# Optimization experiments

Measured on AMD Instinct MI355X. Metric: run time of the kernel, lower is better.

## Reference

```python
import jax, jax.numpy as jnp
import numpy as np

B, S, E, H, D = 4, 2048, 2048, 16, 128
EPS = 1e-6


def _rope_cache(seq_len, dim, base=10000.0):
    # standard rotary cache, half-split layout matching rotate_half
    inv_freq = 1.0 / (base ** (np.arange(0, dim // 2, dtype=np.float32) / (dim // 2)))
    t = np.arange(seq_len, dtype=np.float32)
    freqs = np.outer(t, inv_freq)                     # [S, D/2]
    emb = np.concatenate([freqs, freqs], axis=-1)     # [S, D]
    cos = jnp.asarray(np.cos(emb))[None, :, None, :]  # [1, S, 1, D]
    sin = jnp.asarray(np.sin(emb))[None, :, None, :]
    return cos, sin


def setup_inputs() -> dict:
    key = jax.random.key(0)
    ks = jax.random.split(key, 5)
    scale = 1.0 / np.sqrt(E)
    x = jax.random.normal(ks[0], (B, S, E), dtype=jnp.float32)
    Wq = jax.random.normal(ks[1], (E, E), dtype=jnp.float32) * scale
    Wk = jax.random.normal(ks[2], (E, E), dtype=jnp.float32) * scale
    Wv = jax.random.normal(ks[3], (E, E), dtype=jnp.float32) * scale
    Wo = jax.random.normal(ks[4], (E, E), dtype=jnp.float32) * scale
    cos, sin = _rope_cache(S, D)
    return {"x": x, "cos": cos, "sin": sin, "Wq": Wq, "Wk": Wk, "Wv": Wv, "Wo": Wo}


def _rotate_half(t):
    d = t.shape[-1] // 2
    return jnp.concatenate([-t[..., d:], t[..., :d]], axis=-1)


def _rms_norm(t, eps):
    return t * jax.lax.rsqrt(jnp.mean(t * t, axis=-1, keepdims=True) + eps)


def reference(x, cos, sin, Wq, Wk, Wv, Wo):
    b, s, _ = x.shape
    # QKV projections (Linear without bias: x @ W.T), reshape to heads
    q = (x @ Wq.T).reshape(b, s, H, D)
    k = (x @ Wk.T).reshape(b, s, H, D)
    v = (x @ Wv.T).reshape(b, s, H, D)
    # RoPE then QK RMSNorm (no learned scale)
    q = _rms_norm(q * cos + _rotate_half(q) * sin, EPS)
    k = _rms_norm(k * cos + _rotate_half(k) * sin, EPS)
    # non-causal SDPA
    scores = jnp.einsum("bqhd,bkhd->bhqk", q, k) / np.sqrt(D)
    probs = jax.nn.softmax(scores, axis=-1)
    y = jnp.einsum("bhqk,bkhd->bqhd", probs, v).reshape(b, s, H * D)
    return y @ Wo.T
```

## Files before the change

### kernel.cpp

```cpp
#include <hip/hip_runtime.h>
#include <hip/hip_bf16.h>
#include <math.h>


typedef __bf16 bf16_t;
typedef __bf16 bf16x2 __attribute__((ext_vector_type(2)));
typedef __bf16 bf16x4 __attribute__((ext_vector_type(4)));
typedef __bf16 bf16x8 __attribute__((ext_vector_type(8)));
typedef float f32x2 __attribute__((ext_vector_type(2)));
typedef float f32x4 __attribute__((ext_vector_type(4)));
typedef float f32x16 __attribute__((ext_vector_type(16)));
typedef unsigned int u32;
typedef u32 u32x4 __attribute__((ext_vector_type(4)));

typedef __attribute__((address_space(1))) const void gas_cvoid;
typedef __attribute__((address_space(3))) void las_void;

#define MFMA16(a, b, c) __builtin_amdgcn_mfma_f32_16x16x32_bf16((a), (b), (c), 0, 0, 0)
#define MFMA32(a, b, c) __builtin_amdgcn_mfma_f32_32x32x16_bf16((a), (b), (c), 0, 0, 0)

__device__ __forceinline__ void gload16(const void* g, void* l) {
  __builtin_amdgcn_global_load_lds((gas_cvoid*)g, (las_void*)l, 16, 0, 0);
}
__device__ __forceinline__ void pl32(u32& a, u32& b) {
  asm volatile("v_permlane32_swap_b32 %0, %1" : "+v"(a), "+v"(b));
}
__device__ __forceinline__ float fexp2(float x) {
  float r;
  asm("v_exp_f32 %0, %1" : "=v"(r) : "v"(x));
  return r;
}

__global__ __launch_bounds__(256) void cvt_bf16(const float* __restrict__ in,
                                                bf16_t* __restrict__ out) {
  const size_t i = ((size_t)blockIdx.x * 256 + threadIdx.x) * 4;
  f32x4 v = *(const f32x4*)&in[i];
  bf16x4 o;
#pragma unroll
  for (int j = 0; j < 4; ++j) o[j] = (bf16_t)v[j];
  *(bf16x4*)&out[i] = o;
}
__global__ __launch_bounds__(256) void cvt_w4(const float* __restrict__ w0,
                                              const float* __restrict__ w1,
                                              const float* __restrict__ w2,
                                              const float* __restrict__ w3,
                                              bf16_t* __restrict__ o0,
                                              bf16_t* __restrict__ o1,
                                              bf16_t* __restrict__ o2,
                                              bf16_t* __restrict__ o3) {
  const int which = blockIdx.x >> 12;
  const float* in = which == 0 ? w0 : which == 1 ? w1 : which == 2 ? w2 : w3;
  bf16_t* out = which == 0 ? o0 : which == 1 ? o1 : which == 2 ? o2 : o3;
  const size_t i = ((size_t)(blockIdx.x & 4095) * 256 + threadIdx.x) * 4;
  f32x4 v = *(const f32x4*)&in[i];
  bf16x4 o;
#pragma unroll
  for (int j = 0; j < 4; ++j) o[j] = (bf16_t)v[j];
  *(bf16x4*)&out[i] = o;
}

template <int MODE, typename CT, int NT_T>
__global__ __launch_bounds__(512, 2) void gemm8(const bf16_t* __restrict__ A,
                                                const bf16_t* __restrict__ Bt,
                                                CT* __restrict__ C) {
  constexpr int K = 2048;
  __shared__ __attribute__((aligned(16))) char lds[131072];
  const int tid = threadIdx.x;
  const int wave = tid >> 6, lane = tid & 63;
  const int bid = blockIdx.x;
  const int swz = (bid & 7) * 32 + (bid >> 3);
  const int m0 = (swz / NT_T) * 256, n0 = (swz % NT_T) * 256;

  const int srow = tid >> 3;
  const int scol = ((tid & 7) ^ (srow & 7)) * 8;
  const bf16_t* aBase = A + (size_t)(m0 + srow) * K + scol;
  const bf16_t* bBase = Bt + (size_t)(n0 + srow) * K + scol;

  const int wm = wave >> 2, wn = wave & 3;
  const int l15 = lane & 15, l4 = lane >> 4;
  const int axor = l15 & 7;
  char* const wdst = lds + wave * 1024;

  f32x4 acc[8][4] = {};

  gload16(bBase, wdst + 32768);
  gload16(bBase + (size_t)64 * K, wdst + 32768 + 8192);
  gload16(bBase + (size_t)128 * K, wdst + 32768 + 16384);
  gload16(bBase + (size_t)192 * K, wdst + 32768 + 24576);
  gload16(aBase, wdst);
  gload16(aBase + (size_t)128 * K, wdst + 16384);
  gload16(aBase + (size_t)64 * K, wdst + 8192);
  gload16(aBase + (size_t)192 * K, wdst + 24576);

  for (int t = 0; t < 32; ++t) {
    const int buf = t & 1, nbuf = buf ^ 1;
    const char* la = lds + buf * 65536 + wm * 16384;
    const char* lb = lds + buf * 65536 + 32768 + (wn >> 1) * 16384 + (wn & 1) * 8192;
    char* const ndst = wdst + nbuf * 65536;
    bf16x8 bF[4][2];
#pragma unroll
    for (int q = 0; q < 4; ++q) {
      if (q == 0) {
        asm volatile("s_waitcnt vmcnt(2)" ::: "memory");
      } else if (q == 2) {
        if (t < 31)
          asm volatile("s_waitcnt vmcnt(4)" ::: "memory");
        else
          asm volatile("s_waitcnt vmcnt(0)" ::: "memory");
      }
      __builtin_amdgcn_s_barrier();

      bf16x8 aF[2][2];
#pragma unroll
      for (int dm = 0; dm < 2; ++dm)
#pragma unroll
        for (int kk = 0; kk < 2; ++kk)
          aF[dm][kk] = *(const bf16x8*)(la + ((q * 2 + dm) * 16 + l15) * 128 +
                                        ((kk * 4 + l4) ^ axor) * 16);
      if (q == 0) {
#pragma unroll
        for (int ni = 0; ni < 4; ++ni)
#pragma unroll
          for (int kk = 0; kk < 2; ++kk)
            bF[ni][kk] = *(const bf16x8*)(lb + (ni * 16 + l15) * 128 +
                                          ((kk * 4 + l4) ^ axor) * 16);
      }
      if (t < 31) {
        const int off = (t + 1) * 64;
        if (q == 0) {
          gload16(bBase + off, ndst + 32768);
          gload16(bBase + (size_t)64 * K + off, ndst + 32768 + 8192);
        } else if (q == 1) {
          gload16(bBase + (size_t)128 * K + off, ndst + 32768 + 16384);
          gload16(bBase + (size_t)192 * K + off, ndst + 32768 + 24576);
        } else if (q == 2) {
          gload16(aBase + off, ndst);
          gload16(aBase + (size_t)128 * K + off, ndst + 16384);
        } else {
          gload16(aBase + (size_t)64 * K + off, ndst + 8192);
          gload16(aBase + (size_t)192 * K + off, ndst + 24576);
        }
      }
      __builtin_amdgcn_s_setprio(1);
#pragma unroll
      for (int kk = 0; kk < 2; ++kk)
#pragma unroll
        for (int dm = 0; dm < 2; ++dm)
#pragma unroll
          for (int ni = 0; ni < 4; ++ni)
            acc[q * 2 + dm][ni] = MFMA16(aF[dm][kk], bF[ni][kk], acc[q * 2 + dm][ni]);
      __builtin_amdgcn_s_setprio(0);
    }
  }

  const int rBase = m0 + wm * 128 + l4 * 4;
  const int cBase = n0 + wn * 64 + l15;
#pragma unroll
  for (int mi = 0; mi < 8; ++mi)
#pragma unroll
    for (int ni = 0; ni < 4; ++ni)
#pragma unroll
      for (int j = 0; j < 4; ++j) {
        const int r = rBase + mi * 16 + j;
        const int c = cBase + ni * 16;
        const CT v = (CT)acc[mi][ni][j];
        if (MODE == 0) {
          const int b = r >> 11, s = r & 2047, hh = c >> 7, d = c & 127;
          C[(((size_t)(b * 16 + hh)) * 2048 + s) * 128 + d] = v;
        } else if (MODE == 1) {
          C[(size_t)r * 2048 + c] = v;
        } else {
          const int hh = r >> 7, dd = r & 127, b = c >> 11, s = c & 2047;
          C[((size_t)(b * 16 + hh) * 128 + dd) * 2048 + s] = v;
        }
      }
}

__global__ __launch_bounds__(256) void rope_rms(bf16_t* __restrict__ T,
                                                const float* __restrict__ Cs,
                                                const float* __restrict__ Sn) {
  const int wave = threadIdx.x >> 6, lane = threadIdx.x & 63;
#pragma unroll 1
  for (int rr = 0; rr < 8; ++rr) {
    const size_t row = (size_t)blockIdx.x * 32 + wave * 8 + rr;
    const int s = (int)(row & 2047);
    bf16_t* p = &T[row * 128 + 2 * lane];
    const float a0 = (float)p[0], a1 = (float)p[1];
    f32x2 cv = *(const f32x2*)&Cs[(size_t)s * 128 + 2 * lane];
    f32x2 sv = *(const f32x2*)&Sn[(size_t)s * 128 + 2 * lane];
    const float p0 = __shfl_xor(a0, 32);
    const float p1 = __shfl_xor(a1, 32);
    const float sg = (lane < 32) ? -1.f : 1.f;
    const float r0 = a0 * cv.x + sg * p0 * sv.x;
    const float r1 = a1 * cv.y + sg * p1 * sv.y;
    float ss = r0 * r0 + r1 * r1;
#pragma unroll
    for (int off = 1; off < 64; off <<= 1) ss += __shfl_xor(ss, off);
    const float inv = rsqrtf(ss * (1.0f / 128.0f) + 1e-6f);
    p[0] = (bf16_t)(r0 * inv);
    p[1] = (bf16_t)(r1 * inv);
  }
}

__global__ __launch_bounds__(512, 2) void attn_fwd(const bf16_t* __restrict__ Q,
                                                   const bf16_t* __restrict__ K,
                                                   const bf16_t* __restrict__ Vt,
                                                   bf16_t* __restrict__ Y) {
  __shared__ __attribute__((aligned(16))) bf16_t ldsK[2][64 * 128];
  __shared__ __attribute__((aligned(16))) bf16_t ldsV[2][128 * 64];
  const int tid = threadIdx.x, wave = tid >> 6, lane = tid & 63;
  const int l31 = lane & 31, hi = lane >> 5;
  const int pid = blockIdx.x;
  const int bh = (pid & 7) * 8 + ((pid >> 3) & 7);
  const int qb = pid >> 6;
  const int b = bh >> 4, h = bh & 15;
  const bf16_t* Qh = Q + (size_t)bh * 2048 * 128;
  const bf16_t* Kh = K + (size_t)bh * 2048 * 128;
  const bf16_t* Vh = Vt + (size_t)bh * 128 * 2048;
  const int q0 = qb * 256 + wave * 32;

  bf16x8 qf[8];
#pragma unroll
  for (int dk = 0; dk < 8; ++dk)
    qf[dk] = *(const bf16x8*)&Qh[(size_t)(q0 + l31) * 128 + dk * 16 + hi * 8];

  f32x16 ot[4] = {};
  float l_r = 0.f;
  const float SC2 = 0.08838834764831845f * 1.44269504088896341f;
  const float NC2 = -11.5f * 1.44269504088896341f;

  auto stage = [&](int kt, int bu) {
#pragma unroll
    for (int i = 0; i < 2; ++i) {
      const int G = wave * 64 + lane + i * 512;
      char* dstK = (char*)&ldsK[bu][0] + (wave * 64 + i * 512) * 16;
      char* dstV = (char*)&ldsV[bu][0] + (wave * 64 + i * 512) * 16;
      const int kvr = G >> 4, glk = G & 15;
      gload16(Kh + (size_t)(kt * 64 + kvr) * 128 + ((glk ^ (kvr & 7)) * 8), dstK);
      const int dr = G >> 3, glv = G & 7;
      gload16(Vh + (size_t)dr * 2048 + kt * 64 + ((glv ^ (dr & 7)) * 8), dstV);
    }
  };

  stage(0, 0);
  stage(1, 1);
  asm volatile("s_waitcnt vmcnt(4)" ::: "memory");
  __builtin_amdgcn_s_barrier();
  __builtin_amdgcn_sched_barrier(0);

  for (int kt = 0; kt < 32; ++kt) {
    const int bu = kt & 1;
    const int r7 = l31 & 7;

    f32x16 sa0 = {}, sa1 = {};
    __builtin_amdgcn_s_setprio(1);
#pragma unroll
    for (int dk = 0; dk < 8; ++dk) {
      const int g = ((dk << 1) | hi) ^ r7;
      bf16x8 kf0 = *(const bf16x8*)&ldsK[bu][l31 * 128 + g * 8];
      bf16x8 kf1 = *(const bf16x8*)&ldsK[bu][(32 + l31) * 128 + g * 8];
      sa0 = MFMA32(kf0, qf[dk], sa0);
      sa1 = MFMA32(kf1, qf[dk], sa1);
    }
    __builtin_amdgcn_s_setprio(0);

    u32 w[2][8];
    float ssum = 0.f;
#pragma unroll
    for (int i = 0; i < 8; ++i) {
      const float p0 = fexp2(fmaf(sa0[2 * i], SC2, NC2));
      const float p1 = fexp2(fmaf(sa0[2 * i + 1], SC2, NC2));
      const float p2 = fexp2(fmaf(sa1[2 * i], SC2, NC2));
      const float p3 = fexp2(fmaf(sa1[2 * i + 1], SC2, NC2));
      ssum += (p0 + p1) + (p2 + p3);
      bf16x2 t0, t1;
      t0[0] = (bf16_t)p0; t0[1] = (bf16_t)p1;
      t1[0] = (bf16_t)p2; t1[1] = (bf16_t)p3;
      w[0][i] = __builtin_bit_cast(u32, t0);
      w[1][i] = __builtin_bit_cast(u32, t1);
    }
    ssum += __shfl_xor(ssum, 32);
    l_r += ssum;

#pragma unroll
    for (int ks = 0; ks < 4; ++ks) {
      const int tsel = ks >> 1, k4 = (ks & 1) * 4;
      u32 a0 = w[tsel][k4 + 0], b0 = w[tsel][k4 + 2];
      u32 a1 = w[tsel][k4 + 1], b1 = w[tsel][k4 + 3];
      pl32(a0, b0);
      pl32(a1, b1);
      u32x4 fw;
      fw.x = a0; fw.y = a1; fw.z = b0; fw.w = b1;
      const bf16x8 pf = __builtin_bit_cast(bf16x8, fw);
      const int gv = ((ks << 1) | hi) ^ r7;
      __builtin_amdgcn_s_setprio(1);
#pragma unroll
      for (int db = 0; db < 4; ++db) {
        bf16x8 vf = *(const bf16x8*)&ldsV[bu][(db * 32 + l31) * 64 + gv * 8];
        ot[db] = MFMA32(vf, pf, ot[db]);
      }
      __builtin_amdgcn_s_setprio(0);
    }

    __builtin_amdgcn_s_barrier();
    __builtin_amdgcn_sched_barrier(0);
    if (kt < 30) {
      stage(kt + 2, bu);
      asm volatile("s_waitcnt vmcnt(4)" ::: "memory");
    } else {
      asm volatile("s_waitcnt vmcnt(0)" ::: "memory");
    }
    __builtin_amdgcn_s_barrier();
    __builtin_amdgcn_sched_barrier(0);
  }

  const float rl = 1.f / l_r;
  const size_t yrow = ((size_t)(b * 2048 + q0 + l31) * 16 + h) * 128;
#pragma unroll
  for (int db = 0; db < 4; ++db)
#pragma unroll
    for (int g2 = 0; g2 < 4; ++g2) {
      bf16x4 ov;
#pragma unroll
      for (int j = 0; j < 4; ++j) ov[j] = (bf16_t)(ot[db][g2 * 4 + j] * rl);
      *(bf16x4*)&Y[yrow + db * 32 + g2 * 8 + hi * 4] = ov;
    }
}

extern "C" void kernel_launch(void* const* d_in, const int* in_sizes, int n_in,
                              void* d_out, int out_size, void* d_ws, size_t ws_size,
                              hipStream_t stream) {
  const float* x = (const float*)d_in[0];
  const float* cs = (const float*)d_in[1];
  const float* sn = (const float*)d_in[2];
  const float* Wq = (const float*)d_in[3];
  const float* Wk = (const float*)d_in[4];
  const float* Wv = (const float*)d_in[5];
  const float* Wo = (const float*)d_in[6];

  bf16_t* ws = (bf16_t*)d_ws;
  const size_t TSZ = (size_t)4 * 2048 * 2048;
  const size_t WSZ = (size_t)2048 * 2048;
  bf16_t* xb = ws;
  bf16_t* Wqb = ws + TSZ;
  bf16_t* Wkb = Wqb + WSZ;
  bf16_t* Wvb = Wkb + WSZ;
  bf16_t* Wob = Wvb + WSZ;
  bf16_t* Qb = ws + 2 * TSZ;
  bf16_t* Kb = Qb + TSZ;
  bf16_t* Vtb = Kb + TSZ;
  bf16_t* Yb = xb;

  cvt_bf16<<<16384, 256, 0, stream>>>(x, xb);
  cvt_w4<<<16384, 256, 0, stream>>>(Wq, Wk, Wv, Wo, Wqb, Wkb, Wvb, Wob);

  gemm8<0, bf16_t, 8><<<256, 512, 0, stream>>>(xb, Wqb, Qb);
  gemm8<0, bf16_t, 8><<<256, 512, 0, stream>>>(xb, Wkb, Kb);
  gemm8<2, bf16_t, 32><<<256, 512, 0, stream>>>(Wvb, xb, Vtb);
  rope_rms<<<4096, 256, 0, stream>>>(Qb, cs, sn);
  rope_rms<<<4096, 256, 0, stream>>>(Kb, cs, sn);
  attn_fwd<<<512, 512, 0, stream>>>(Qb, Kb, Vtb, Yb);
  gemm8<1, float, 8><<<256, 512, 0, stream>>>(Yb, Wob, (float*)d_out);
}
```

Baseline: 476.3 us.

## Process two query tiles per attention block and fuse the Q/K RoPE launches

The attention kernel now gives each wave two 32-row query tiles, 256 rows apart. It reuses every K and V fragment read from LDS for both tiles and halves the grid to 256 blocks of 512 threads. This halves the global-to-LDS K/V staging traffic and LDS reads per unit of work. The cost is roughly double the accumulator and Q registers, and the min-blocks launch bound is dropped, so each CU runs fewer resident waves to hide latency. Separately, the two RoPE+RMSNorm launches are merged into one launch with an 8192-block grid that picks Q or K by block index, saving one kernel launch.

```diff
diff --git a/kernel.cpp b/kernel.cpp
--- a/kernel.cpp
+++ b/kernel.cpp
@@ -176,13 +176,16 @@
       }
 }
 
-__global__ __launch_bounds__(256) void rope_rms(bf16_t* __restrict__ T,
-                                                const float* __restrict__ Cs,
-                                                const float* __restrict__ Sn) {
+__global__ __launch_bounds__(256) void rope_rms2(bf16_t* __restrict__ Qb,
+                                                 bf16_t* __restrict__ Kb,
+                                                 const float* __restrict__ Cs,
+                                                 const float* __restrict__ Sn) {
+  bf16_t* T = (blockIdx.x >> 12) ? Kb : Qb;
+  const int bid = blockIdx.x & 4095;
   const int wave = threadIdx.x >> 6, lane = threadIdx.x & 63;
 #pragma unroll 1
   for (int rr = 0; rr < 8; ++rr) {
-    const size_t row = (size_t)blockIdx.x * 32 + wave * 8 + rr;
+    const size_t row = (size_t)bid * 32 + wave * 8 + rr;
     const int s = (int)(row & 2047);
     bf16_t* p = &T[row * 128 + 2 * lane];
     const float a0 = (float)p[0], a1 = (float)p[1];
@@ -202,10 +205,10 @@
   }
 }
 
-__global__ __launch_bounds__(512, 2) void attn_fwd(const bf16_t* __restrict__ Q,
-                                                   const bf16_t* __restrict__ K,
-                                                   const bf16_t* __restrict__ Vt,
-                                                   bf16_t* __restrict__ Y) {
+__global__ __launch_bounds__(512) void attn_fwd(const bf16_t* __restrict__ Q,
+                                                const bf16_t* __restrict__ K,
+                                                const bf16_t* __restrict__ Vt,
+                                                bf16_t* __restrict__ Y) {
   __shared__ __attribute__((aligned(16))) bf16_t ldsK[2][64 * 128];
   __shared__ __attribute__((aligned(16))) bf16_t ldsV[2][128 * 64];
   const int tid = threadIdx.x, wave = tid >> 6, lane = tid & 63;
@@ -217,15 +220,17 @@
   const bf16_t* Qh = Q + (size_t)bh * 2048 * 128;
   const bf16_t* Kh = K + (size_t)bh * 2048 * 128;
   const bf16_t* Vh = Vt + (size_t)bh * 128 * 2048;
-  const int q0 = qb * 256 + wave * 32;
-
-  bf16x8 qf[8];
-#pragma unroll
-  for (int dk = 0; dk < 8; ++dk)
-    qf[dk] = *(const bf16x8*)&Qh[(size_t)(q0 + l31) * 128 + dk * 16 + hi * 8];
-
-  f32x16 ot[4] = {};
-  float l_r = 0.f;
+  const int q0 = qb * 512 + wave * 32;
+
+  bf16x8 qfA[8], qfB[8];
+#pragma unroll
+  for (int dk = 0; dk < 8; ++dk) {
+    qfA[dk] = *(const bf16x8*)&Qh[(size_t)(q0 + l31) * 128 + dk * 16 + hi * 8];
+    qfB[dk] = *(const bf16x8*)&Qh[(size_t)(q0 + 256 + l31) * 128 + dk * 16 + hi * 8];
+  }
+
+  f32x16 otA[4] = {}, otB[4] = {};
+  float lA = 0.f, lB = 0.f;
   const float SC2 = 0.08838834764831845f * 1.44269504088896341f;
   const float NC2 = -11.5f * 1.44269504088896341f;
 
@@ -252,52 +257,77 @@
     const int bu = kt & 1;
     const int r7 = l31 & 7;
 
-    f32x16 sa0 = {}, sa1 = {};
+    f32x16 sa0A = {}, sa1A = {}, sa0B = {}, sa1B = {};
     __builtin_amdgcn_s_setprio(1);
 #pragma unroll
     for (int dk = 0; dk < 8; ++dk) {
       const int g = ((dk << 1) | hi) ^ r7;
       bf16x8 kf0 = *(const bf16x8*)&ldsK[bu][l31 * 128 + g * 8];
       bf16x8 kf1 = *(const bf16x8*)&ldsK[bu][(32 + l31) * 128 + g * 8];
-      sa0 = MFMA32(kf0, qf[dk], sa0);
-      sa1 = MFMA32(kf1, qf[dk], sa1);
+      sa0A = MFMA32(kf0, qfA[dk], sa0A);
+      sa1A = MFMA32(kf1, qfA[dk], sa1A);
+      sa0B = MFMA32(kf0, qfB[dk], sa0B);
+      sa1B = MFMA32(kf1, qfB[dk], sa1B);
     }
     __builtin_amdgcn_s_setprio(0);
 
-    u32 w[2][8];
-    float ssum = 0.f;
+    u32 wA[2][8], wB[2][8];
+    float ssA = 0.f, ssB = 0.f;
 #pragma unroll
     for (int i = 0; i < 8; ++i) {
-      const float p0 = fexp2(fmaf(sa0[2 * i], SC2, NC2));
-      const float p1 = fexp2(fmaf(sa0[2 * i + 1], SC2, NC2));
-      const float p2 = fexp2(fmaf(sa1[2 * i], SC2, NC2));
-      const float p3 = fexp2(fmaf(sa1[2 * i + 1], SC2, NC2));
-      ssum += (p0 + p1) + (p2 + p3);
+      const float p0 = fexp2(fmaf(sa0A[2 * i], SC2, NC2));
+      const float p1 = fexp2(fmaf(sa0A[2 * i + 1], SC2, NC2));
+      const float p2 = fexp2(fmaf(sa1A[2 * i], SC2, NC2));
+      const float p3 = fexp2(fmaf(sa1A[2 * i + 1], SC2, NC2));
+      ssA += (p0 + p1) + (p2 + p3);
       bf16x2 t0, t1;
       t0[0] = (bf16_t)p0; t0[1] = (bf16_t)p1;
       t1[0] = (bf16_t)p2; t1[1] = (bf16_t)p3;
-      w[0][i] = __builtin_bit_cast(u32, t0);
-      w[1][i] = __builtin_bit_cast(u32, t1);
-    }
-    ssum += __shfl_xor(ssum, 32);
-    l_r += ssum;
+      wA[0][i] = __builtin_bit_cast(u32, t0);
+      wA[1][i] = __builtin_bit_cast(u32, t1);
+    }
+#pragma unroll
+    for (int i = 0; i < 8; ++i) {
+      const float p0 = fexp2(fmaf(sa0B[2 * i], SC2, NC2));
+      const float p1 = fexp2(fmaf(sa0B[2 * i + 1], SC2, NC2));
+      const float p2 = fexp2(fmaf(sa1B[2 * i], SC2, NC2));
+      const float p3 = fexp2(fmaf(sa1B[2 * i + 1], SC2, NC2));
+      ssB += (p0 + p1) + (p2 + p3);
+      bf16x2 t0, t1;
+      t0[0] = (bf16_t)p0; t0[1] = (bf16_t)p1;
+      t1[0] = (bf16_t)p2; t1[1] = (bf16_t)p3;
+      wB[0][i] = __builtin_bit_cast(u32, t0);
+      wB[1][i] = __builtin_bit_cast(u32, t1);
+    }
+    ssA += __shfl_xor(ssA, 32);
+    ssB += __shfl_xor(ssB, 32);
+    lA += ssA;
+    lB += ssB;
 
 #pragma unroll
     for (int ks = 0; ks < 4; ++ks) {
       const int tsel = ks >> 1, k4 = (ks & 1) * 4;
-      u32 a0 = w[tsel][k4 + 0], b0 = w[tsel][k4 + 2];
-      u32 a1 = w[tsel][k4 + 1], b1 = w[tsel][k4 + 3];
+      u32 a0 = wA[tsel][k4 + 0], b0 = wA[tsel][k4 + 2];
+      u32 a1 = wA[tsel][k4 + 1], b1 = wA[tsel][k4 + 3];
       pl32(a0, b0);
       pl32(a1, b1);
-      u32x4 fw;
-      fw.x = a0; fw.y = a1; fw.z = b0; fw.w = b1;
-      const bf16x8 pf = __builtin_bit_cast(bf16x8, fw);
+      u32x4 fwA;
+      fwA.x = a0; fwA.y = a1; fwA.z = b0; fwA.w = b1;
+      const bf16x8 pfA = __builtin_bit_cast(bf16x8, fwA);
+      u32 c0 = wB[tsel][k4 + 0], d0 = wB[tsel][k4 + 2];
+      u32 c1 = wB[tsel][k4 + 1], d1 = wB[tsel][k4 + 3];
+      pl32(c0, d0);
+      pl32(c1, d1);
+      u32x4 fwB;
+      fwB.x = c0; fwB.y = c1; fwB.z = d0; fwB.w = d1;
+      const bf16x8 pfB = __builtin_bit_cast(bf16x8, fwB);
       const int gv = ((ks << 1) | hi) ^ r7;
       __builtin_amdgcn_s_setprio(1);
 #pragma unroll
       for (int db = 0; db < 4; ++db) {
         bf16x8 vf = *(const bf16x8*)&ldsV[bu][(db * 32 + l31) * 64 + gv * 8];
-        ot[db] = MFMA32(vf, pf, ot[db]);
+        otA[db] = MFMA32(vf, pfA, otA[db]);
+        otB[db] = MFMA32(vf, pfB, otB[db]);
       }
       __builtin_amdgcn_s_setprio(0);
     }
@@ -314,16 +344,21 @@
     __builtin_amdgcn_sched_barrier(0);
   }
 
-  const float rl = 1.f / l_r;
-  const size_t yrow = ((size_t)(b * 2048 + q0 + l31) * 16 + h) * 128;
+  const float rlA = 1.f / lA, rlB = 1.f / lB;
+  const size_t yrA = ((size_t)(b * 2048 + q0 + l31) * 16 + h) * 128;
+  const size_t yrB = ((size_t)(b * 2048 + q0 + 256 + l31) * 16 + h) * 128;
 #pragma unroll
   for (int db = 0; db < 4; ++db)
 #pragma unroll
     for (int g2 = 0; g2 < 4; ++g2) {
-      bf16x4 ov;
-#pragma unroll
-      for (int j = 0; j < 4; ++j) ov[j] = (bf16_t)(ot[db][g2 * 4 + j] * rl);
-      *(bf16x4*)&Y[yrow + db * 32 + g2 * 8 + hi * 4] = ov;
+      bf16x4 ovA, ovB;
+#pragma unroll
+      for (int j = 0; j < 4; ++j) {
+        ovA[j] = (bf16_t)(otA[db][g2 * 4 + j] * rlA);
+        ovB[j] = (bf16_t)(otB[db][g2 * 4 + j] * rlB);
+      }
+      *(bf16x4*)&Y[yrA + db * 32 + g2 * 8 + hi * 4] = ovA;
+      *(bf16x4*)&Y[yrB + db * 32 + g2 * 8 + hi * 4] = ovB;
     }
 }
 
@@ -357,8 +392,7 @@
   gemm8<0, bf16_t, 8><<<256, 512, 0, stream>>>(xb, Wqb, Qb);
   gemm8<0, bf16_t, 8><<<256, 512, 0, stream>>>(xb, Wkb, Kb);
   gemm8<2, bf16_t, 32><<<256, 512, 0, stream>>>(Wvb, xb, Vtb);
-  rope_rms<<<4096, 256, 0, stream>>>(Qb, cs, sn);
-  rope_rms<<<4096, 256, 0, stream>>>(Kb, cs, sn);
-  attn_fwd<<<512, 512, 0, stream>>>(Qb, Kb, Vtb, Yb);
+  rope_rms2<<<8192, 256, 0, stream>>>(Qb, Kb, cs, sn);
+  attn_fwd<<<256, 512, 0, stream>>>(Qb, Kb, Vtb, Yb);
   gemm8<1, float, 8><<<256, 512, 0, stream>>>(Yb, Wob, (float*)d_out);
 }
```

Result: slower. 749.6 us (+57.4%).

## Switch GEMM to 32x32x16 MFMA tiles and merge Q/K rope kernels

Applied to the files above, without the earlier changes.

Each wave of the GEMM now computes its 128x64 tile with 32x32x16 bf16 MFMA instructions (4x2 f32x16 accumulators) in place of 16x16x32 ones. LDS fragment loads and the epilogue index mapping are rewritten to match the 32-row lane layout. The larger instruction should cut issue overhead and LDS fragment reads per FLOP, at the cost of a different epilogue store pattern. The two rope_rms launches for Q and K are also merged into one 8192-block launch to save a kernel launch.

```diff
diff --git a/kernel.cpp b/kernel.cpp
--- a/kernel.cpp
+++ b/kernel.cpp
@@ -16,7 +16,6 @@
 typedef __attribute__((address_space(1))) const void gas_cvoid;
 typedef __attribute__((address_space(3))) void las_void;
 
-#define MFMA16(a, b, c) __builtin_amdgcn_mfma_f32_16x16x32_bf16((a), (b), (c), 0, 0, 0)
 #define MFMA32(a, b, c) __builtin_amdgcn_mfma_f32_32x32x16_bf16((a), (b), (c), 0, 0, 0)
 
 __device__ __forceinline__ void gload16(const void* g, void* l) {
@@ -77,11 +76,11 @@
   const bf16_t* bBase = Bt + (size_t)(n0 + srow) * K + scol;
 
   const int wm = wave >> 2, wn = wave & 3;
-  const int l15 = lane & 15, l4 = lane >> 4;
-  const int axor = l15 & 7;
+  const int l31 = lane & 31, hi = lane >> 5;
+  const int axor = l31 & 7;
   char* const wdst = lds + wave * 1024;
 
-  f32x4 acc[8][4] = {};
+  f32x16 acc[4][2] = {};
 
   gload16(bBase, wdst + 32768);
   gload16(bBase + (size_t)64 * K, wdst + 32768 + 8192);
@@ -97,7 +96,7 @@
     const char* la = lds + buf * 65536 + wm * 16384;
     const char* lb = lds + buf * 65536 + 32768 + (wn >> 1) * 16384 + (wn & 1) * 8192;
     char* const ndst = wdst + nbuf * 65536;
-    bf16x8 bF[4][2];
+    bf16x8 bF[2][4];
 #pragma unroll
     for (int q = 0; q < 4; ++q) {
       if (q == 0) {
@@ -110,20 +109,18 @@
       }
       __builtin_amdgcn_s_barrier();
 
-      bf16x8 aF[2][2];
-#pragma unroll
-      for (int dm = 0; dm < 2; ++dm)
-#pragma unroll
-        for (int kk = 0; kk < 2; ++kk)
-          aF[dm][kk] = *(const bf16x8*)(la + ((q * 2 + dm) * 16 + l15) * 128 +
-                                        ((kk * 4 + l4) ^ axor) * 16);
+      bf16x8 aF[4];
+#pragma unroll
+      for (int kk = 0; kk < 4; ++kk)
+        aF[kk] = *(const bf16x8*)(la + (q * 32 + l31) * 128 +
+                                  ((kk * 2 + hi) ^ axor) * 16);
       if (q == 0) {
 #pragma unroll
-        for (int ni = 0; ni < 4; ++ni)
-#pragma unroll
-          for (int kk = 0; kk < 2; ++kk)
-            bF[ni][kk] = *(const bf16x8*)(lb + (ni * 16 + l15) * 128 +
-                                          ((kk * 4 + l4) ^ axor) * 16);
+        for (int nt = 0; nt < 2; ++nt)
+#pragma unroll
+          for (int kk = 0; kk < 4; ++kk)
+            bF[nt][kk] = *(const bf16x8*)(lb + (nt * 32 + l31) * 128 +
+                                          ((kk * 2 + hi) ^ axor) * 16);
       }
       if (t < 31) {
         const int off = (t + 1) * 64;
@@ -143,27 +140,25 @@
       }
       __builtin_amdgcn_s_setprio(1);
 #pragma unroll
-      for (int kk = 0; kk < 2; ++kk)
-#pragma unroll
-        for (int dm = 0; dm < 2; ++dm)
-#pragma unroll
-          for (int ni = 0; ni < 4; ++ni)
-            acc[q * 2 + dm][ni] = MFMA16(aF[dm][kk], bF[ni][kk], acc[q * 2 + dm][ni]);
+      for (int kk = 0; kk < 4; ++kk)
+#pragma unroll
+        for (int nt = 0; nt < 2; ++nt)
+          acc[q][nt] = MFMA32(aF[kk], bF[nt][kk], acc[q][nt]);
       __builtin_amdgcn_s_setprio(0);
     }
   }
 
-  const int rBase = m0 + wm * 128 + l4 * 4;
-  const int cBase = n0 + wn * 64 + l15;
-#pragma unroll
-  for (int mi = 0; mi < 8; ++mi)
-#pragma unroll
-    for (int ni = 0; ni < 4; ++ni)
-#pragma unroll
-      for (int j = 0; j < 4; ++j) {
-        const int r = rBase + mi * 16 + j;
-        const int c = cBase + ni * 16;
-        const CT v = (CT)acc[mi][ni][j];
+  const int rBase = m0 + wm * 128 + 4 * hi;
+  const int cBase = n0 + wn * 64 + l31;
+#pragma unroll
+  for (int mt = 0; mt < 4; ++mt)
+#pragma unroll
+    for (int nt = 0; nt < 2; ++nt)
+#pragma unroll
+      for (int j = 0; j < 16; ++j) {
+        const int r = rBase + mt * 32 + (j & 3) + 8 * (j >> 2);
+        const int c = cBase + nt * 32;
+        const CT v = (CT)acc[mt][nt][j];
         if (MODE == 0) {
           const int b = r >> 11, s = r & 2047, hh = c >> 7, d = c & 127;
           C[(((size_t)(b * 16 + hh)) * 2048 + s) * 128 + d] = v;
@@ -176,13 +171,16 @@
       }
 }
 
-__global__ __launch_bounds__(256) void rope_rms(bf16_t* __restrict__ T,
-                                                const float* __restrict__ Cs,
-                                                const float* __restrict__ Sn) {
+__global__ __launch_bounds__(256) void rope_rms2(bf16_t* __restrict__ Qb,
+                                                 bf16_t* __restrict__ Kb,
+                                                 const float* __restrict__ Cs,
+                                                 const float* __restrict__ Sn) {
+  bf16_t* T = (blockIdx.x >> 12) ? Kb : Qb;
+  const int bid = blockIdx.x & 4095;
   const int wave = threadIdx.x >> 6, lane = threadIdx.x & 63;
 #pragma unroll 1
   for (int rr = 0; rr < 8; ++rr) {
-    const size_t row = (size_t)blockIdx.x * 32 + wave * 8 + rr;
+    const size_t row = (size_t)bid * 32 + wave * 8 + rr;
     const int s = (int)(row & 2047);
     bf16_t* p = &T[row * 128 + 2 * lane];
     const float a0 = (float)p[0], a1 = (float)p[1];
@@ -357,8 +355,7 @@
   gemm8<0, bf16_t, 8><<<256, 512, 0, stream>>>(xb, Wqb, Qb);
   gemm8<0, bf16_t, 8><<<256, 512, 0, stream>>>(xb, Wkb, Kb);
   gemm8<2, bf16_t, 32><<<256, 512, 0, stream>>>(Wvb, xb, Vtb);
-  rope_rms<<<4096, 256, 0, stream>>>(Qb, cs, sn);
-  rope_rms<<<4096, 256, 0, stream>>>(Kb, cs, sn);
+  rope_rms2<<<8192, 256, 0, stream>>>(Qb, Kb, cs, sn);
   attn_fwd<<<512, 512, 0, stream>>>(Qb, Kb, Vtb, Yb);
   gemm8<1, float, 8><<<256, 512, 0, stream>>>(Yb, Wob, (float*)d_out);
 }
```

Measured after the change: 502.4 us. 5.5% more time.

## Fuse RoPE+RMSNorm into Q/K GEMM epilogue and merge conversion kernels

Applied to the files above, without the earlier changes.

The Q and K projection GEMMs now stage their bf16 tile in LDS and apply RoPE and RMS normalization per head row before writing out, which removes the two standalone rope_rms passes that re-read and re-wrote Q and K. The x and weight fp32-to-bf16 conversions are merged into a single launch. Together these cut global memory traffic and launch overhead. The cost is a longer GEMM epilogue that serializes over 64 rows per wave, with extra LDS syncs.

```diff
diff --git a/kernel.cpp b/kernel.cpp
--- a/kernel.cpp
+++ b/kernel.cpp
@@ -31,27 +31,28 @@
   return r;
 }
 
-__global__ __launch_bounds__(256) void cvt_bf16(const float* __restrict__ in,
-                                                bf16_t* __restrict__ out) {
-  const size_t i = ((size_t)blockIdx.x * 256 + threadIdx.x) * 4;
-  f32x4 v = *(const f32x4*)&in[i];
-  bf16x4 o;
-#pragma unroll
-  for (int j = 0; j < 4; ++j) o[j] = (bf16_t)v[j];
-  *(bf16x4*)&out[i] = o;
-}
-__global__ __launch_bounds__(256) void cvt_w4(const float* __restrict__ w0,
-                                              const float* __restrict__ w1,
-                                              const float* __restrict__ w2,
-                                              const float* __restrict__ w3,
-                                              bf16_t* __restrict__ o0,
-                                              bf16_t* __restrict__ o1,
-                                              bf16_t* __restrict__ o2,
-                                              bf16_t* __restrict__ o3) {
-  const int which = blockIdx.x >> 12;
-  const float* in = which == 0 ? w0 : which == 1 ? w1 : which == 2 ? w2 : w3;
-  bf16_t* out = which == 0 ? o0 : which == 1 ? o1 : which == 2 ? o2 : o3;
-  const size_t i = ((size_t)(blockIdx.x & 4095) * 256 + threadIdx.x) * 4;
+__global__ __launch_bounds__(256) void cvt_all(const float* __restrict__ x,
+                                               const float* __restrict__ w0,
+                                               const float* __restrict__ w1,
+                                               const float* __restrict__ w2,
+                                               const float* __restrict__ w3,
+                                               bf16_t* __restrict__ xo,
+                                               bf16_t* __restrict__ o0,
+                                               bf16_t* __restrict__ o1,
+                                               bf16_t* __restrict__ o2,
+                                               bf16_t* __restrict__ o3) {
+  const float* in;
+  bf16_t* out;
+  size_t i;
+  if (blockIdx.x < 16384) {
+    in = x; out = xo;
+    i = ((size_t)blockIdx.x * 256 + threadIdx.x) * 4;
+  } else {
+    const int which = (blockIdx.x - 16384) >> 12;
+    in = which == 0 ? w0 : which == 1 ? w1 : which == 2 ? w2 : w3;
+    out = which == 0 ? o0 : which == 1 ? o1 : which == 2 ? o2 : o3;
+    i = ((size_t)((blockIdx.x - 16384) & 4095) * 256 + threadIdx.x) * 4;
+  }
   f32x4 v = *(const f32x4*)&in[i];
   bf16x4 o;
 #pragma unroll
@@ -62,7 +63,9 @@
 template <int MODE, typename CT, int NT_T>
 __global__ __launch_bounds__(512, 2) void gemm8(const bf16_t* __restrict__ A,
                                                 const bf16_t* __restrict__ Bt,
-                                                CT* __restrict__ C) {
+                                                CT* __restrict__ C,
+                                                const float* __restrict__ Cs,
+                                                const float* __restrict__ Sn) {
   constexpr int K = 2048;
   __shared__ __attribute__((aligned(16))) char lds[131072];
   const int tid = threadIdx.x;
@@ -153,6 +156,48 @@
     }
   }
 
+  if (MODE == 3) {
+    __syncthreads();
+    bf16_t* ct = (bf16_t*)lds;
+    const int lrow0 = wm * 128 + l4 * 4;
+    const int lcol0 = wn * 64 + l15;
+#pragma unroll
+    for (int mi = 0; mi < 8; ++mi)
+#pragma unroll
+      for (int ni = 0; ni < 4; ++ni)
+#pragma unroll
+        for (int j = 0; j < 4; ++j)
+          ct[(lrow0 + mi * 16 + j) * 256 + lcol0 + ni * 16] = (bf16_t)acc[mi][ni][j];
+    __syncthreads();
+#pragma unroll 1
+    for (int it = 0; it < 64; ++it) {
+      const int item = wave * 64 + it;
+      const int lr = item >> 1, hl = item & 1;
+      const int r = m0 + lr;
+      const int s = r & 2047, b = r >> 11;
+      const int hh = (n0 >> 7) + hl;
+      const u32 qw = *(const u32*)&ct[lr * 256 + hl * 128 + 2 * lane];
+      const bf16x2 qv = __builtin_bit_cast(bf16x2, qw);
+      const float a0 = (float)qv[0], a1 = (float)qv[1];
+      f32x2 cv = *(const f32x2*)&Cs[(size_t)s * 128 + 2 * lane];
+      f32x2 sv = *(const f32x2*)&Sn[(size_t)s * 128 + 2 * lane];
+      const float p0 = __shfl_xor(a0, 32);
+      const float p1 = __shfl_xor(a1, 32);
+      const float sg = (lane < 32) ? -1.f : 1.f;
+      const float r0 = a0 * cv.x + sg * p0 * sv.x;
+      const float r1 = a1 * cv.y + sg * p1 * sv.y;
+      float ss = r0 * r0 + r1 * r1;
+#pragma unroll
+      for (int off = 1; off < 64; off <<= 1) ss += __shfl_xor(ss, off);
+      const float inv = rsqrtf(ss * (1.0f / 128.0f) + 1e-6f);
+      bf16x2 o;
+      o[0] = (bf16_t)(r0 * inv);
+      o[1] = (bf16_t)(r1 * inv);
+      *(bf16x2*)&((bf16_t*)C)[(((size_t)(b * 16 + hh)) * 2048 + s) * 128 + 2 * lane] = o;
+    }
+    return;
+  }
+
   const int rBase = m0 + wm * 128 + l4 * 4;
   const int cBase = n0 + wn * 64 + l15;
 #pragma unroll
@@ -174,32 +219,6 @@
           C[((size_t)(b * 16 + hh) * 128 + dd) * 2048 + s] = v;
         }
       }
-}
-
-__global__ __launch_bounds__(256) void rope_rms(bf16_t* __restrict__ T,
-                                                const float* __restrict__ Cs,
-                                                const float* __restrict__ Sn) {
-  const int wave = threadIdx.x >> 6, lane = threadIdx.x & 63;
-#pragma unroll 1
-  for (int rr = 0; rr < 8; ++rr) {
-    const size_t row = (size_t)blockIdx.x * 32 + wave * 8 + rr;
-    const int s = (int)(row & 2047);
-    bf16_t* p = &T[row * 128 + 2 * lane];
-    const float a0 = (float)p[0], a1 = (float)p[1];
-    f32x2 cv = *(const f32x2*)&Cs[(size_t)s * 128 + 2 * lane];
-    f32x2 sv = *(const f32x2*)&Sn[(size_t)s * 128 + 2 * lane];
-    const float p0 = __shfl_xor(a0, 32);
-    const float p1 = __shfl_xor(a1, 32);
-    const float sg = (lane < 32) ? -1.f : 1.f;
-    const float r0 = a0 * cv.x + sg * p0 * sv.x;
-    const float r1 = a1 * cv.y + sg * p1 * sv.y;
-    float ss = r0 * r0 + r1 * r1;
-#pragma unroll
-    for (int off = 1; off < 64; off <<= 1) ss += __shfl_xor(ss, off);
-    const float inv = rsqrtf(ss * (1.0f / 128.0f) + 1e-6f);
-    p[0] = (bf16_t)(r0 * inv);
-    p[1] = (bf16_t)(r1 * inv);
-  }
 }
 
 __global__ __launch_bounds__(512, 2) void attn_fwd(const bf16_t* __restrict__ Q,
@@ -351,14 +370,11 @@
   bf16_t* Vtb = Kb + TSZ;
   bf16_t* Yb = xb;
 
-  cvt_bf16<<<16384, 256, 0, stream>>>(x, xb);
-  cvt_w4<<<16384, 256, 0, stream>>>(Wq, Wk, Wv, Wo, Wqb, Wkb, Wvb, Wob);
-
-  gemm8<0, bf16_t, 8><<<256, 512, 0, stream>>>(xb, Wqb, Qb);
-  gemm8<0, bf16_t, 8><<<256, 512, 0, stream>>>(xb, Wkb, Kb);
-  gemm8<2, bf16_t, 32><<<256, 512, 0, stream>>>(Wvb, xb, Vtb);
-  rope_rms<<<4096, 256, 0, stream>>>(Qb, cs, sn);
-  rope_rms<<<4096, 256, 0, stream>>>(Kb, cs, sn);
+  cvt_all<<<32768, 256, 0, stream>>>(x, Wq, Wk, Wv, Wo, xb, Wqb, Wkb, Wvb, Wob);
+
+  gemm8<3, bf16_t, 8><<<256, 512, 0, stream>>>(xb, Wqb, Qb, cs, sn);
+  gemm8<3, bf16_t, 8><<<256, 512, 0, stream>>>(xb, Wkb, Kb, cs, sn);
+  gemm8<2, bf16_t, 32><<<256, 512, 0, stream>>>(Wvb, xb, Vtb, nullptr, nullptr);
   attn_fwd<<<512, 512, 0, stream>>>(Qb, Kb, Vtb, Yb);
-  gemm8<1, float, 8><<<256, 512, 0, stream>>>(Yb, Wob, (float*)d_out);
-}
+  gemm8<1, float, 8><<<256, 512, 0, stream>>>(Yb, Wob, (float*)d_out, nullptr, nullptr);
+}
```

Measured after the change: 498.1 us. 1.05x slower.
